# Kernel tuning notes

Hardware: AMD Instinct MI355X
Metric: run time of the kernel (lower is better)

## Reference

```python
import jax, jax.numpy as jnp
from jax import lax
import numpy as np

B, T, D, H, O, L = 64, 1024, 256, 512, 256, 2


def setup_inputs() -> dict:
    key = jax.random.key(0)
    ks = jax.random.split(key, 12)
    s_in = 1.0 / np.sqrt(H)
    inp = {
        "x": jax.random.normal(ks[0], (B, T, D), dtype=jnp.float32),
        "W_ih0": jax.random.uniform(ks[1], (H, D), jnp.float32, -s_in, s_in),
        "W_hh0": jax.random.uniform(ks[2], (H, H), jnp.float32, -s_in, s_in),
        "b_ih0": jax.random.uniform(ks[3], (H,), jnp.float32, -s_in, s_in),
        "b_hh0": jax.random.uniform(ks[4], (H,), jnp.float32, -s_in, s_in),
        "W_ih1": jax.random.uniform(ks[5], (H, H), jnp.float32, -s_in, s_in),
        "W_hh1": jax.random.uniform(ks[6], (H, H), jnp.float32, -s_in, s_in),
        "b_ih1": jax.random.uniform(ks[7], (H,), jnp.float32, -s_in, s_in),
        "b_hh1": jax.random.uniform(ks[8], (H,), jnp.float32, -s_in, s_in),
        "W_fc": jax.random.uniform(ks[9], (O, H), jnp.float32, -s_in, s_in),
        "b_fc": jax.random.uniform(ks[10], (O,), jnp.float32, -s_in, s_in),
    }
    return inp


def _rnn_layer(inp, W_ih, W_hh, b_ih, b_hh):
    # inp: [B, T, Din] -> outputs [B, T, H], final hidden [B, H]
    # PyTorch: h_t = tanh(x_t @ W_ih^T + b_ih + h_{t-1} @ W_hh^T + b_hh)
    xW = jnp.einsum("btd,hd->bth", inp, W_ih) + b_ih + b_hh  # precompute input proj

    def step(h, xw_t):
        h = jnp.tanh(xw_t + h @ W_hh.T)
        return h, h

    h0 = jnp.zeros((inp.shape[0], W_hh.shape[0]), dtype=inp.dtype)
    hT, hs = lax.scan(step, h0, jnp.swapaxes(xW, 0, 1))  # scan over time
    return jnp.swapaxes(hs, 0, 1), hT


def reference(x, W_ih0, W_hh0, b_ih0, b_hh0, W_ih1, W_hh1, b_ih1, b_hh1, W_fc, b_fc):
    out0, _ = _rnn_layer(x, W_ih0, W_hh0, b_ih0, b_hh0)
    _, hT1 = _rnn_layer(out0, W_ih1, W_hh1, b_ih1, b_hh1)
    # fc applied to hn[-1] (last layer final hidden state)
    return hT1 @ W_fc.T + b_fc  # [B, O]
```

## Files before the change

### kernel.cpp

```cpp
#include <hip/hip_runtime.h>
#include <cmath>


#define Bdim 64
#define Tdim 1024
#define Ddim 256
#define Hdim 512
#define Odim 256

template <int K>
__global__ __launch_bounds__(1024) void gemm_rows(const float* A, const float* W,
                                                  const float* __restrict__ bias_a,
                                                  const float* __restrict__ bias_b,
                                                  float* C) {
  constexpr int KT = 16;
  __shared__ __align__(16) float As[64][KT];
  __shared__ __align__(16) float Ws[KT][516];
  const int t = threadIdx.x;
  const size_t row0 = (size_t)blockIdx.x * 64;
  const int tn = t & 127;
  const int tm = t >> 7;

  float acc[8][4];
#pragma unroll
  for (int i = 0; i < 8; ++i)
#pragma unroll
    for (int j = 0; j < 4; ++j) acc[i][j] = 0.f;

  const int r_st = t >> 4;
  const int k_st = t & 15;

  for (int k0 = 0; k0 < K; k0 += KT) {
    As[r_st][k_st] = A[(row0 + r_st) * K + k0 + k_st];
#pragma unroll
    for (int rep = 0; rep < 8; ++rep) {
      const int idx = rep * 1024 + t;
      const int n = idx >> 4;
      const int kk = idx & 15;
      Ws[kk][n] = W[(size_t)n * K + k0 + kk];
    }
    __syncthreads();
#pragma unroll
    for (int kk = 0; kk < KT; ++kk) {
      float a[8];
#pragma unroll
      for (int i = 0; i < 8; ++i) a[i] = As[tm * 8 + i][kk];
      const float4 w = *(const float4*)&Ws[kk][tn * 4];
#pragma unroll
      for (int i = 0; i < 8; ++i) {
        acc[i][0] = fmaf(a[i], w.x, acc[i][0]);
        acc[i][1] = fmaf(a[i], w.y, acc[i][1]);
        acc[i][2] = fmaf(a[i], w.z, acc[i][2]);
        acc[i][3] = fmaf(a[i], w.w, acc[i][3]);
      }
    }
    __syncthreads();
  }
  float bn[4];
#pragma unroll
  for (int j = 0; j < 4; ++j) bn[j] = bias_a[tn * 4 + j] + bias_b[tn * 4 + j];
#pragma unroll
  for (int i = 0; i < 8; ++i) {
    float4 v;
    v.x = acc[i][0] + bn[0];
    v.y = acc[i][1] + bn[1];
    v.z = acc[i][2] + bn[2];
    v.w = acc[i][3] + bn[3];
    *(float4*)&C[(row0 + tm * 8 + i) * (size_t)Hdim + tn * 4] = v;
  }
}

__device__ __forceinline__ float fast_tanh(float y) {
  const float e2 = __expf(2.0f * y);
  return 1.0f - 2.0f * __builtin_amdgcn_rcpf(e2 + 1.0f);
}

__device__ __forceinline__ unsigned ld_l2_sc0(const unsigned* p) {
  unsigned v;
  asm volatile("global_load_dword %0, %1, off sc0\n\ts_waitcnt vmcnt(0)"
               : "=v"(v)
               : "v"(p)
               : "memory");
  return v;
}
__device__ __forceinline__ void st_l2(unsigned* p, unsigned v) {
  asm volatile("global_store_dword %0, %1, off" ::"v"(p), "v"(v) : "memory");
}

__global__ __launch_bounds__(512, 2) void rnn_scan_coop(
    float* xw,
    const float* __restrict__ Whh,
    unsigned* hbuf,
    unsigned* fbuf,
    float* h_final,
    const int store_seq) {
  const int bi = blockIdx.x;
  const int b = bi & 63;
  const int q = bi >> 6;
  const int t = threadIdx.x;
  const int w = t >> 6;
  const int l = t & 63;
  const int jg0 = q * 128 + 2 * l;
  const bool is_epi = ((w >> 1) == q);

  __shared__ __align__(16) float hL[2][Hdim];
  __shared__ __align__(16) float red[2][8][128];

  float4 W0[16], W1[16];
  {
    const float4* w0p = (const float4*)(Whh + (size_t)jg0 * Hdim + w * 64);
    const float4* w1p = (const float4*)(Whh + (size_t)(jg0 + 1) * Hdim + w * 64);
#pragma unroll
    for (int c = 0; c < 16; ++c) {
      W0[c] = w0p[c];
      W1[c] = w1p[c];
    }
  }
#pragma unroll
  for (int c = 0; c < 16; ++c) {
    asm volatile("" : "+v"(W0[c].x), "+v"(W0[c].y), "+v"(W0[c].z), "+v"(W0[c].w));
    asm volatile("" : "+v"(W1[c].x), "+v"(W1[c].y), "+v"(W1[c].z), "+v"(W1[c].w));
  }

  hL[0][t] = 0.0f;
  __syncthreads();

  float* row = xw + (size_t)b * Tdim * Hdim;
  unsigned* hb_row = hbuf + b * Hdim;
  unsigned* fb_row = fbuf + b * Hdim;
  float xv = is_epi ? row[t] : 0.f;

  for (int s = 0; s < Tdim; ++s, row += Hdim) {
    const int sp = s & 1;

    if (s > 0 && !is_epi) {
      const size_t off = (size_t)((s - 1) & 1) * (Bdim * Hdim) + t;
      const unsigned want = 1024u | ((unsigned)s & 1023u);
      const unsigned* fp = fb_row + off;
      const unsigned* sp_ = hb_row + off;
      unsigned v = ld_l2_sc0(fp);
      if ((v & 2047u) != want) {
        for (;;) {
          v = __hip_atomic_load(sp_, __ATOMIC_RELAXED, __HIP_MEMORY_SCOPE_AGENT);
          if ((v & 2047u) == want) break;
          v = ld_l2_sc0(fp);
          if ((v & 2047u) == want) break;
        }
      }
      hL[sp][t] = __uint_as_float(v & 0xFFFFF800u);
    }

    const float4* h4 = (const float4*)&hL[sp][w * 64];
    float a0 = 0.f, a0b = 0.f, a1 = 0.f, a1b = 0.f;
#pragma unroll
    for (int c = 0; c < 16; ++c) {
      const float4 hv = h4[c];
      a0  = fmaf(W0[c].x, hv.x, a0);
      a0b = fmaf(W0[c].y, hv.y, a0b);
      a0  = fmaf(W0[c].z, hv.z, a0);
      a0b = fmaf(W0[c].w, hv.w, a0b);
      a1  = fmaf(W1[c].x, hv.x, a1);
      a1b = fmaf(W1[c].y, hv.y, a1b);
      a1  = fmaf(W1[c].z, hv.z, a1);
      a1b = fmaf(W1[c].w, hv.w, a1b);
    }
    *(float2*)&red[sp][w][2 * l] = make_float2(a0 + a0b, a1 + a1b);
    __syncthreads();

    if (is_epi) {
      const int e = t & 127;
      float y = xv;
#pragma unroll
      for (int w8 = 0; w8 < 8; ++w8) y += red[sp][w8][e];
      const float hn = fast_tanh(y);
      const unsigned bits = (__float_as_uint(hn) + 0x400u) & 0xFFFFF800u;
      const float hq = __uint_as_float(bits);
      const unsigned pv = bits | 1024u | ((unsigned)(s + 1) & 1023u);
      const size_t off = (size_t)sp * (Bdim * Hdim) + t;
      st_l2(fb_row + off, pv);
      __hip_atomic_store(hb_row + off, pv, __ATOMIC_RELAXED,
                         __HIP_MEMORY_SCOPE_AGENT);
      hL[sp ^ 1][t] = hq;
      if (store_seq) row[t] = hq;
      if (s + 1 < Tdim)
        xv = row[Hdim + t];
      else if (h_final != nullptr)
        h_final[(size_t)b * Hdim + t] = hq;
    }
  }
}

__global__ __launch_bounds__(256) void fc_kernel(const float* __restrict__ h,
                                                 const float* __restrict__ Wfc,
                                                 const float* __restrict__ bfc,
                                                 float* __restrict__ out) {
  __shared__ float hs[Hdim];
  const int b = blockIdx.x, o = threadIdx.x;
  hs[o] = h[(size_t)b * Hdim + o];
  hs[o + 256] = h[(size_t)b * Hdim + 256 + o];
  __syncthreads();
  float acc = bfc[o];
  const float* wr = Wfc + (size_t)o * Hdim;
#pragma unroll 4
  for (int k = 0; k < Hdim; k += 4) {
    const float4 w = *(const float4*)(wr + k);
    acc = fmaf(w.x, hs[k], acc);
    acc = fmaf(w.y, hs[k + 1], acc);
    acc = fmaf(w.z, hs[k + 2], acc);
    acc = fmaf(w.w, hs[k + 3], acc);
  }
  out[(size_t)b * Odim + o] = acc;
}

extern "C" void kernel_launch(void* const* d_in, const int* in_sizes, int n_in,
                              void* d_out, int out_size, void* d_ws, size_t ws_size,
                              hipStream_t stream) {
  const float* x = (const float*)d_in[0];
  const float* W_ih0 = (const float*)d_in[1];
  const float* W_hh0 = (const float*)d_in[2];
  const float* b_ih0 = (const float*)d_in[3];
  const float* b_hh0 = (const float*)d_in[4];
  const float* W_ih1 = (const float*)d_in[5];
  const float* W_hh1 = (const float*)d_in[6];
  const float* b_ih1 = (const float*)d_in[7];
  const float* b_hh1 = (const float*)d_in[8];
  const float* W_fc = (const float*)d_in[9];
  const float* b_fc = (const float*)d_in[10];
  float* out = (float*)d_out;

  float* A = (float*)d_ws;
  unsigned* hbuf0 = (unsigned*)(A + (size_t)Bdim * Tdim * Hdim);
  unsigned* hbuf1 = hbuf0 + (size_t)2 * Bdim * Hdim;
  unsigned* fbuf0 = hbuf1 + (size_t)2 * Bdim * Hdim;
  unsigned* fbuf1 = fbuf0 + (size_t)2 * Bdim * Hdim;
  float* hT1 = (float*)(fbuf1 + (size_t)2 * Bdim * Hdim);

  gemm_rows<Ddim><<<(Bdim * Tdim) / 64, 1024, 0, stream>>>(x, W_ih0, b_ih0, b_hh0, A);

  {
    float* xwp = A;
    const float* W = W_hh0;
    unsigned* hb = hbuf0;
    unsigned* fb = fbuf0;
    float* hf = nullptr;
    int ss = 1;
    void* args[] = {&xwp, (void*)&W, &hb, &fb, &hf, &ss};
    hipLaunchCooperativeKernel((void*)rnn_scan_coop, dim3(Bdim * 4), dim3(512),
                               args, 0, stream);
  }

  gemm_rows<Hdim><<<(Bdim * Tdim) / 64, 1024, 0, stream>>>(A, W_ih1, b_ih1, b_hh1, A);

  {
    float* xwp = A;
    const float* W = W_hh1;
    unsigned* hb = hbuf1;
    unsigned* fb = fbuf1;
    float* hf = hT1;
    int ss = 0;
    void* args[] = {&xwp, (void*)&W, &hb, &fb, &hf, &ss};
    hipLaunchCooperativeKernel((void*)rnn_scan_coop, dim3(Bdim * 4), dim3(512),
                               args, 0, stream);
  }

  fc_kernel<<<Bdim, Odim, 0, stream>>>(hT1, W_fc, b_fc, out);
}
```

Baseline: 3.713 ms.

## Remove block barrier from RNN scan by per-wave reduction and vectorized polling

Restructures the recurrent step so each wave owns 16 hidden outputs and splits the K dimension across 4 lane groups, reducing with cross-lane shuffles instead of a shared-memory reduction plus __syncthreads. Every wave now polls the full hidden vector itself using 8-dword vector loads per lane with wave-wide all-checks, falling back to an sc0 sc1 load path. Each wave holds a private shared-memory copy of h and handles its own tanh and publish, which removes the block-wide barrier and the dedicated epilogue waves. The cost is redundant global polling traffic from all waves, with each block reading all 512 hidden values per step.

```diff
diff --git a/kernel.cpp b/kernel.cpp
--- a/kernel.cpp
+++ b/kernel.cpp
@@ -75,13 +75,25 @@
   return 1.0f - 2.0f * __builtin_amdgcn_rcpf(e2 + 1.0f);
 }
 
-__device__ __forceinline__ unsigned ld_l2_sc0(const unsigned* p) {
-  unsigned v;
-  asm volatile("global_load_dword %0, %1, off sc0\n\ts_waitcnt vmcnt(0)"
-               : "=v"(v)
-               : "v"(p)
-               : "memory");
-  return v;
+typedef unsigned uv4 __attribute__((ext_vector_type(4)));
+
+__device__ __forceinline__ void ld8_l2(const unsigned* p, uv4& a, uv4& b) {
+  asm volatile(
+      "global_load_dwordx4 %0, %2, off sc0\n\t"
+      "global_load_dwordx4 %1, %2, off offset:16 sc0\n\t"
+      "s_waitcnt vmcnt(0)"
+      : "=&v"(a), "=&v"(b)
+      : "v"(p)
+      : "memory");
+}
+__device__ __forceinline__ void ld8_mall(const unsigned* p, uv4& a, uv4& b) {
+  asm volatile(
+      "global_load_dwordx4 %0, %2, off sc0 sc1\n\t"
+      "global_load_dwordx4 %1, %2, off offset:16 sc0 sc1\n\t"
+      "s_waitcnt vmcnt(0)"
+      : "=&v"(a), "=&v"(b)
+      : "v"(p)
+      : "memory");
 }
 __device__ __forceinline__ void st_l2(unsigned* p, unsigned v) {
   asm volatile("global_store_dword %0, %1, off" ::"v"(p), "v"(v) : "memory");
@@ -100,93 +112,117 @@
   const int t = threadIdx.x;
   const int w = t >> 6;
   const int l = t & 63;
-  const int jg0 = q * 128 + 2 * l;
-  const bool is_epi = ((w >> 1) == q);
-
-  __shared__ __align__(16) float hL[2][Hdim];
-  __shared__ __align__(16) float red[2][8][128];
-
-  float4 W0[16], W1[16];
+  const int lj = l & 15;
+  const int g = l >> 4;
+  const int j = q * 128 + w * 16 + lj;
+  const int ks0 = g * 128;
+
+  __shared__ __align__(16) float hS[8][4 * 132];
+  float* hw = hS[w];
+  const int hww = g * 132 + 8 * lj;
+  float* const hrd = &hw[g * 132];
+
+  float4 Wr[32];
   {
-    const float4* w0p = (const float4*)(Whh + (size_t)jg0 * Hdim + w * 64);
-    const float4* w1p = (const float4*)(Whh + (size_t)(jg0 + 1) * Hdim + w * 64);
-#pragma unroll
-    for (int c = 0; c < 16; ++c) {
-      W0[c] = w0p[c];
-      W1[c] = w1p[c];
-    }
-  }
-#pragma unroll
-  for (int c = 0; c < 16; ++c) {
-    asm volatile("" : "+v"(W0[c].x), "+v"(W0[c].y), "+v"(W0[c].z), "+v"(W0[c].w));
-    asm volatile("" : "+v"(W1[c].x), "+v"(W1[c].y), "+v"(W1[c].z), "+v"(W1[c].w));
-  }
-
-  hL[0][t] = 0.0f;
-  __syncthreads();
+    const float4* wp = (const float4*)(Whh + (size_t)j * Hdim + ks0);
+#pragma unroll
+    for (int c = 0; c < 32; ++c) Wr[c] = wp[c];
+  }
+#pragma unroll
+  for (int c = 0; c < 32; ++c)
+    asm volatile("" : "+v"(Wr[c].x), "+v"(Wr[c].y), "+v"(Wr[c].z), "+v"(Wr[c].w));
+
+  *(float4*)&hw[hww] = make_float4(0.f, 0.f, 0.f, 0.f);
+  *(float4*)&hw[hww + 4] = make_float4(0.f, 0.f, 0.f, 0.f);
 
   float* row = xw + (size_t)b * Tdim * Hdim;
   unsigned* hb_row = hbuf + b * Hdim;
   unsigned* fb_row = fbuf + b * Hdim;
-  float xv = is_epi ? row[t] : 0.f;
+  float xv = row[j];
 
   for (int s = 0; s < Tdim; ++s, row += Hdim) {
     const int sp = s & 1;
 
-    if (s > 0 && !is_epi) {
-      const size_t off = (size_t)((s - 1) & 1) * (Bdim * Hdim) + t;
+    if (s > 0) {
+      const size_t off = (size_t)(sp ^ 1) * (Bdim * Hdim) + 8 * l;
       const unsigned want = 1024u | ((unsigned)s & 1023u);
       const unsigned* fp = fb_row + off;
-      const unsigned* sp_ = hb_row + off;
-      unsigned v = ld_l2_sc0(fp);
-      if ((v & 2047u) != want) {
+      const unsigned* mp = hb_row + off;
+      uv4 a, bb;
+      ld8_l2(fp, a, bb);
+      int ok = ((a.x & 2047u) == want) & ((a.y & 2047u) == want) &
+               ((a.z & 2047u) == want) & ((a.w & 2047u) == want) &
+               ((bb.x & 2047u) == want) & ((bb.y & 2047u) == want) &
+               ((bb.z & 2047u) == want) & ((bb.w & 2047u) == want);
+      if (!__all(ok)) {
         for (;;) {
-          v = __hip_atomic_load(sp_, __ATOMIC_RELAXED, __HIP_MEMORY_SCOPE_AGENT);
-          if ((v & 2047u) == want) break;
-          v = ld_l2_sc0(fp);
-          if ((v & 2047u) == want) break;
+          ld8_mall(mp, a, bb);
+          ok = ((a.x & 2047u) == want) & ((a.y & 2047u) == want) &
+               ((a.z & 2047u) == want) & ((a.w & 2047u) == want) &
+               ((bb.x & 2047u) == want) & ((bb.y & 2047u) == want) &
+               ((bb.z & 2047u) == want) & ((bb.w & 2047u) == want);
+          if (__all(ok)) break;
+          ld8_l2(fp, a, bb);
+          ok = ((a.x & 2047u) == want) & ((a.y & 2047u) == want) &
+               ((a.z & 2047u) == want) & ((a.w & 2047u) == want) &
+               ((bb.x & 2047u) == want) & ((bb.y & 2047u) == want) &
+               ((bb.z & 2047u) == want) & ((bb.w & 2047u) == want);
+          if (__all(ok)) break;
         }
       }
-      hL[sp][t] = __uint_as_float(v & 0xFFFFF800u);
-    }
-
-    const float4* h4 = (const float4*)&hL[sp][w * 64];
-    float a0 = 0.f, a0b = 0.f, a1 = 0.f, a1b = 0.f;
-#pragma unroll
-    for (int c = 0; c < 16; ++c) {
-      const float4 hv = h4[c];
-      a0  = fmaf(W0[c].x, hv.x, a0);
-      a0b = fmaf(W0[c].y, hv.y, a0b);
-      a0  = fmaf(W0[c].z, hv.z, a0);
-      a0b = fmaf(W0[c].w, hv.w, a0b);
-      a1  = fmaf(W1[c].x, hv.x, a1);
-      a1b = fmaf(W1[c].y, hv.y, a1b);
-      a1  = fmaf(W1[c].z, hv.z, a1);
-      a1b = fmaf(W1[c].w, hv.w, a1b);
-    }
-    *(float2*)&red[sp][w][2 * l] = make_float2(a0 + a0b, a1 + a1b);
-    __syncthreads();
-
-    if (is_epi) {
-      const int e = t & 127;
-      float y = xv;
-#pragma unroll
-      for (int w8 = 0; w8 < 8; ++w8) y += red[sp][w8][e];
-      const float hn = fast_tanh(y);
-      const unsigned bits = (__float_as_uint(hn) + 0x400u) & 0xFFFFF800u;
-      const float hq = __uint_as_float(bits);
-      const unsigned pv = bits | 1024u | ((unsigned)(s + 1) & 1023u);
-      const size_t off = (size_t)sp * (Bdim * Hdim) + t;
-      st_l2(fb_row + off, pv);
-      __hip_atomic_store(hb_row + off, pv, __ATOMIC_RELAXED,
+      const unsigned M = 0xFFFFF800u;
+      *(float4*)&hw[hww] =
+          make_float4(__uint_as_float(a.x & M), __uint_as_float(a.y & M),
+                      __uint_as_float(a.z & M), __uint_as_float(a.w & M));
+      *(float4*)&hw[hww + 4] =
+          make_float4(__uint_as_float(bb.x & M), __uint_as_float(bb.y & M),
+                      __uint_as_float(bb.z & M), __uint_as_float(bb.w & M));
+    }
+
+    const float4* h4 = (const float4*)hrd;
+    float s0 = 0.f, s1 = 0.f, s2 = 0.f, s3 = 0.f;
+#pragma unroll
+    for (int c = 0; c < 32; c += 4) {
+      const float4 h0 = h4[c + 0];
+      const float4 h1 = h4[c + 1];
+      const float4 h2 = h4[c + 2];
+      const float4 h3 = h4[c + 3];
+      s0 = fmaf(Wr[c + 0].x, h0.x, s0);
+      s0 = fmaf(Wr[c + 0].y, h0.y, s0);
+      s0 = fmaf(Wr[c + 0].z, h0.z, s0);
+      s0 = fmaf(Wr[c + 0].w, h0.w, s0);
+      s1 = fmaf(Wr[c + 1].x, h1.x, s1);
+      s1 = fmaf(Wr[c + 1].y, h1.y, s1);
+      s1 = fmaf(Wr[c + 1].z, h1.z, s1);
+      s1 = fmaf(Wr[c + 1].w, h1.w, s1);
+      s2 = fmaf(Wr[c + 2].x, h2.x, s2);
+      s2 = fmaf(Wr[c + 2].y, h2.y, s2);
+      s2 = fmaf(Wr[c + 2].z, h2.z, s2);
+      s2 = fmaf(Wr[c + 2].w, h2.w, s2);
+      s3 = fmaf(Wr[c + 3].x, h3.x, s3);
+      s3 = fmaf(Wr[c + 3].y, h3.y, s3);
+      s3 = fmaf(Wr[c + 3].z, h3.z, s3);
+      s3 = fmaf(Wr[c + 3].w, h3.w, s3);
+    }
+    float y = (s0 + s1) + (s2 + s3);
+    y += __shfl_xor(y, 16, 64);
+    y += __shfl_xor(y, 32, 64);
+    y += xv;
+
+    const float hn = fast_tanh(y);
+    const unsigned bits = (__float_as_uint(hn) + 0x400u) & 0xFFFFF800u;
+    const float hq = __uint_as_float(bits);
+    const unsigned pv = bits | 1024u | ((unsigned)(s + 1) & 1023u);
+    const size_t offp = (size_t)sp * (Bdim * Hdim) + j;
+    if (l < 16) {
+      st_l2(fb_row + offp, pv);
+      __hip_atomic_store(hb_row + offp, pv, __ATOMIC_RELAXED,
                          __HIP_MEMORY_SCOPE_AGENT);
-      hL[sp ^ 1][t] = hq;
-      if (store_seq) row[t] = hq;
-      if (s + 1 < Tdim)
-        xv = row[Hdim + t];
-      else if (h_final != nullptr)
-        h_final[(size_t)b * Hdim + t] = hq;
-    }
+      if (store_seq) row[j] = hq;
+      if (s + 1 == Tdim && h_final != nullptr)
+        h_final[(size_t)b * Hdim + j] = hq;
+    }
+    if (s + 1 < Tdim) xv = row[Hdim + j];
   }
 }
 
```

Result: slower. 5.369 ms (+44.6%).
